# Kernel optimization log

Measured on AMD Instinct MI355X. Metric: run time of the kernel, lower is better.

The kernel has to match this reference:

```python
import jax, jax.numpy as jnp
import numpy as np

B_, C, N, M, DX = 4, 8, 1024, 1024, 1
POINTS_PER_UNIT = 64


def setup_inputs() -> dict:
    key = jax.random.key(0)
    k1, k2, k3 = jax.random.split(key, 3)
    xz = jax.random.uniform(k1, (M, DX), dtype=jnp.float32)          # grid locations
    z = jax.random.normal(k2, (B_, C, M, M), dtype=jnp.float32)      # grid encoding
    x = jax.random.normal(k3, (B_, N, DX), dtype=jnp.float32)        # target locations
    log_scale = jnp.log(jnp.float32(2.0 / POINTS_PER_UNIT))          # learned scalar
    return {"xz": xz, "z": z, "x": x, "log_scale": log_scale}


def reference(xz, z, x, log_scale):
    # pairwise squared distances: (b, n, m)
    dists2 = jnp.sum((x[:, :, None, :] - xz[None, None, :, :]) ** 2, axis=-1)
    # RBF weights
    weights = jnp.exp(-0.5 * dists2 / jnp.exp(2.0 * log_scale))      # (b, n, m)
    # weighted interpolation of grid encoding: (b, c, n, m)
    z1 = jnp.einsum("bnm,bcmk->bcnk", weights, z)
    # outer product z1 @ z1^T: (b, c, n, n)
    z2 = jnp.einsum("bcnk,bcok->bcno", z1, z1)
    return (xz, z2)
```

## Files before the change

kernel.cpp:

```cpp
#include <hip/hip_runtime.h>
#include <hip/hip_bf16.h>


typedef __attribute__((ext_vector_type(8))) unsigned short u16x8;
typedef __attribute__((ext_vector_type(8))) __bf16 bf16x8;
typedef __attribute__((ext_vector_type(4))) float f32x4;

typedef __attribute__((address_space(1))) void gvoid;
typedef __attribute__((address_space(3))) void svoid;
#define GLDS(g, s) __builtin_amdgcn_global_load_lds((gvoid*)(g), (svoid*)(s), 16, 0, 0)
#define BAR() asm volatile("s_barrier" ::: "memory")

__device__ __forceinline__ unsigned short f2bf(float f) {
  unsigned int u = __builtin_bit_cast(unsigned int, f);
  u += 0x7fffu + ((u >> 16) & 1u);
  return (unsigned short)(u >> 16);
}

__device__ __forceinline__ bf16x8 as_bf16x8(u16x8 v) {
  return __builtin_bit_cast(bf16x8, v);
}

__global__ void weights_kernel(const float* __restrict__ xz, const float* __restrict__ x,
                               const float* __restrict__ ls, unsigned short* __restrict__ W) {
  int bn = blockIdx.x;
  float xv = x[bn];
  float coef = -0.5f * __expf(-2.0f * ls[0]);
  unsigned short* Wrow = W + (size_t)bn * 1024;
  #pragma unroll
  for (int i = 0; i < 4; ++i) {
    int m = threadIdx.x + i * 256;
    float d = xv - xz[m];
    Wrow[m] = f2bf(__expf(coef * d * d));
  }
}

__global__ void transpose_kernel(const float* __restrict__ Z, unsigned short* __restrict__ Zt) {
  __shared__ float tile[64][65];
  int bc = blockIdx.z;
  const float* Zp = Z + ((size_t)bc << 20);
  unsigned short* Ztp = Zt + ((size_t)bc << 20);
  int m0 = blockIdx.x * 64, k0 = blockIdx.y * 64;
  int tx = threadIdx.x & 63, tg = threadIdx.x >> 6;
  #pragma unroll
  for (int i = 0; i < 16; ++i) {
    int ml = tg + i * 4;
    tile[ml][tx] = Zp[(size_t)(m0 + ml) * 1024 + k0 + tx];
  }
  __syncthreads();
  int tx2 = (threadIdx.x & 31) * 2, kg = threadIdx.x >> 5;
  #pragma unroll
  for (int i = 0; i < 8; ++i) {
    int kl = kg + i * 8;
    ushort2 v;
    v.x = f2bf(tile[tx2][kl]);
    v.y = f2bf(tile[tx2 + 1][kl]);
    *(ushort2*)&Ztp[(size_t)(k0 + kl) * 1024 + m0 + tx2] = v;
  }
}

template<bool A_PER_B>
__global__ __launch_bounds__(512, 2)
void gemm_nt8(const unsigned short* __restrict__ A, const unsigned short* __restrict__ B,
              unsigned short* __restrict__ Cbf) {
  extern __shared__ __align__(16) char smem[];

  const int bid = blockIdx.x;
  const int w = ((bid & 7) << 6) + (bid >> 3);
  const int bc = w >> 4;
  const int t  = w & 15;
  const int bi = t & 3, bj = t >> 2;

  const unsigned short* Ap = A + ((size_t)(A_PER_B ? (bc >> 3) : bc) << 20);
  const unsigned short* Bp = B + ((size_t)bc << 20);
  const int tid = threadIdx.x;
  const int wv = tid >> 6, lane = tid & 63;
  const int wr = wv >> 2, wc = wv & 3;
  const int la = lane & 15, ha = lane >> 4;

  f32x4 acc[8][4] = {};

  const int slog = (lane & 7) ^ (lane >> 3);
  const int rloc = 2 * (lane >> 3) + (slog & 1);
  const int cloc = (slog >> 1) * 8;
  const unsigned short* gA0 = Ap + (size_t)(bi*256 +       wv*16 + rloc) * 1024 + cloc;
  const unsigned short* gA1 = Ap + (size_t)(bi*256 + 128 + wv*16 + rloc) * 1024 + cloc;
  const unsigned short* gB0 = Bp + (size_t)(bj*256 +       wv*16 + rloc) * 1024 + cloc;
  const unsigned short* gB1 = Bp + (size_t)(bj*256 + 128 + wv*16 + rloc) * 1024 + cloc;
  const int ldsw = wv * 1024;

  auto stageA = [&](int d, int kh, int kt) {
    const int ko = kt * 64 + kh * 32;
    char* dst = smem + d * 32768 + kh * 16384 + ldsw;
    GLDS(gA0 + ko, dst); GLDS(gA1 + ko, dst + 8192);
  };
  auto stageB = [&](int d, int kh, int kt) {
    const int ko = kt * 64 + kh * 32;
    char* dst = smem + 65536 + d * 32768 + kh * 16384 + ldsw;
    GLDS(gB0 + ko, dst); GLDS(gB1 + ko, dst + 8192);
  };

  const int sphys = ((ha << 1) | (la & 1)) ^ (la >> 1);
  const int abase = wr * 8192 + (la >> 1) * 128 + sphys * 16;
  const int bbase = 65536 + wc * 4096 + (la >> 1) * 128 + sphys * 16;

  u16x8 af[4], bfr[4];
  auto lda = [&](int d, int kh, int ms) {
    const char* p = smem + d * 32768 + kh * 16384 + ms * 4096 + abase;
    af[0] = *(const u16x8*)(p);
    af[1] = *(const u16x8*)(p + 1024);
    af[2] = *(const u16x8*)(p + 2048);
    af[3] = *(const u16x8*)(p + 3072);
  };
  auto ldb = [&](int d, int kh) {
    const char* p = smem + d * 32768 + kh * 16384 + bbase;
    bfr[0] = *(const u16x8*)(p);
    bfr[1] = *(const u16x8*)(p + 1024);
    bfr[2] = *(const u16x8*)(p + 2048);
    bfr[3] = *(const u16x8*)(p + 3072);
  };
  auto mfma16 = [&](int ms) {
    __builtin_amdgcn_s_setprio(1);
    #pragma unroll
    for (int i = 0; i < 4; ++i)
      #pragma unroll
      for (int n = 0; n < 4; ++n)
        acc[ms * 4 + i][n] = __builtin_amdgcn_mfma_f32_16x16x32_bf16(
            as_bf16x8(af[i]), as_bf16x8(bfr[n]), acc[ms * 4 + i][n], 0, 0, 0);
    __builtin_amdgcn_s_setprio(0);
  };

  stageA(0, 0, 0); stageB(0, 0, 0);
  stageA(0, 1, 0); stageB(0, 1, 0);
  stageA(1, 0, 1); stageB(1, 0, 1);
  asm volatile("s_waitcnt vmcnt(8)" ::: "memory");
  BAR();

  for (int tt = 0; tt < 16; ++tt) {
    const int d = tt & 1;
    if (tt < 15) stageA(d ^ 1, 1, tt + 1);
    ldb(d, 0); lda(d, 0, 0);
    BAR(); mfma16(0); BAR();
    if (tt < 15) stageB(d ^ 1, 1, tt + 1);
    lda(d, 0, 1);
    BAR(); mfma16(1);
    if (tt < 15) { asm volatile("s_waitcnt vmcnt(8)" ::: "memory"); }
    else         { asm volatile("s_waitcnt vmcnt(0)" ::: "memory"); }
    BAR();
    if (tt < 14) stageA(d, 0, tt + 2);
    ldb(d, 1); lda(d, 1, 0);
    BAR(); mfma16(0); BAR();
    if (tt < 14) stageB(d, 0, tt + 2);
    lda(d, 1, 1);
    BAR(); mfma16(1);
    if (tt < 14)       { asm volatile("s_waitcnt vmcnt(8)" ::: "memory"); }
    else if (tt == 14) { asm volatile("s_waitcnt vmcnt(4)" ::: "memory"); }
    BAR();
  }

  const size_t cb20 = (size_t)bc << 20;
  unsigned short* sE = (unsigned short*)(smem) + wv * 1152;
  const int r2 = lane >> 2, ch = lane & 3;
  #pragma unroll
  for (int mb = 0; mb < 8; ++mb) {
    #pragma unroll
    for (int nb = 0; nb < 4; ++nb)
      #pragma unroll
      for (int j = 0; j < 4; ++j)
        sE[(ha * 4 + j) * 72 + nb * 16 + la] = f2bf(acc[mb][nb][j]);
    u16x8 v0 = *(const u16x8*)&sE[r2 * 72 + ch * 16];
    u16x8 v1 = *(const u16x8*)&sE[r2 * 72 + ch * 16 + 8];
    unsigned short* gp = Cbf + cb20 +
        (size_t)(bi * 256 + wr * 128 + mb * 16 + r2) * 1024 + bj * 256 + wc * 64 + ch * 16;
    *(u16x8*)gp = v0;
    *(u16x8*)(gp + 8) = v1;
  }
}

__global__ __launch_bounds__(256, 3)
void gemm2_sym(const unsigned short* __restrict__ A, float* __restrict__ Cf) {
  __shared__ __align__(16) char smem[49152];

  const int chunk = 144;
  int w = ((int)blockIdx.x & 7) * chunk + ((int)blockIdx.x >> 3);
  int bc = w / 36;
  int t  = w % 36;
  int bi = 0;
  while (t >= 8 - bi) { t -= 8 - bi; ++bi; }
  int bj = bi + t;

  const unsigned short* Ap = A + ((size_t)bc << 20);
  const int tid = threadIdx.x;
  const int wave = tid >> 6, lane = tid & 63;
  const int wr = wave >> 1, wc = wave & 1;
  const int la = lane & 15, ha = lane >> 4;
  f32x4 acc[4][4] = {};

  const int slog = (lane & 7) ^ ((lane >> 3) & 7);
  const int rloc = 2 * (lane >> 3) + (slog & 1);
  const int cloc = (slog >> 1) * 8;
  const unsigned short* gA0 = Ap + (size_t)(bi * 128 + (wave * 2)     * 16 + rloc) * 1024 + cloc;
  const unsigned short* gA1 = Ap + (size_t)(bi * 128 + (wave * 2 + 1) * 16 + rloc) * 1024 + cloc;
  const unsigned short* gB0 = Ap + (size_t)(bj * 128 + (wave * 2)     * 16 + rloc) * 1024 + cloc;
  const unsigned short* gB1 = Ap + (size_t)(bj * 128 + (wave * 2 + 1) * 16 + rloc) * 1024 + cloc;

  auto stage = [&](int slot, int kt) {
    char* dA = smem + slot * 8192 + wave * 2048;
    char* dB = smem + 24576 + slot * 8192 + wave * 2048;
    GLDS(gA0 + kt, dA); GLDS(gA1 + kt, dA + 1024);
    GLDS(gB0 + kt, dB); GLDS(gB1 + kt, dB + 1024);
  };

  const int sphys = ((ha << 1) | (la & 1)) ^ (la >> 1);
  const int aoff = wr * 4096 + (la >> 1) * 128 + sphys * 16;
  const int boff = wc * 4096 + (la >> 1) * 128 + sphys * 16;

  auto compute = [&](int slot) {
    const char* rA = smem + slot * 8192;
    const char* rB = smem + 24576 + slot * 8192;
    u16x8 af[4], bfr[4];
    #pragma unroll
    for (int m = 0; m < 4; ++m) af[m]  = *(const u16x8*)(rA + aoff + m * 1024);
    #pragma unroll
    for (int n = 0; n < 4; ++n) bfr[n] = *(const u16x8*)(rB + boff + n * 1024);
    #pragma unroll
    for (int m = 0; m < 4; ++m)
      #pragma unroll
      for (int n = 0; n < 4; ++n)
        acc[m][n] = __builtin_amdgcn_mfma_f32_16x16x32_bf16(
            as_bf16x8(af[m]), as_bf16x8(bfr[n]), acc[m][n], 0, 0, 0);
  };

  stage(0, 0);
  stage(1, 32);
  asm volatile("s_waitcnt vmcnt(4)" ::: "memory");
  __builtin_amdgcn_s_barrier();
  int sl0 = 0, sl1 = 1, sl2 = 2;
  for (int t2 = 0; t2 < 32; ++t2) {
    if (t2 < 30) stage(sl2, (t2 + 2) * 32);
    compute(sl0);
    if (t2 < 30)       asm volatile("s_waitcnt vmcnt(4)" ::: "memory");
    else if (t2 == 30) asm volatile("s_waitcnt vmcnt(0)" ::: "memory");
    if (t2 < 31) __builtin_amdgcn_s_barrier();
    int tmp = sl0; sl0 = sl1; sl1 = sl2; sl2 = tmp;
  }
  __builtin_amdgcn_s_barrier();

  const size_t cb20 = (size_t)bc << 20;

  #pragma unroll
  for (int m = 0; m < 4; ++m) {
    int row0 = bi * 128 + wr * 64 + m * 16 + ha * 4;
    #pragma unroll
    for (int n = 0; n < 4; ++n) {
      int col = bj * 128 + wc * 64 + n * 16 + la;
      #pragma unroll
      for (int j = 0; j < 4; ++j)
        Cf[cb20 + (size_t)(row0 + j) * 1024 + col] = acc[m][n][j];
    }
  }
  if (bi != bj) {
    float (*sT)[129] = (float(*)[129])smem;
    #pragma unroll
    for (int b = 0; b < 4; ++b) {
      if (wr == (b >> 1)) {
        #pragma unroll
        for (int dm = 0; dm < 2; ++dm) {
          int m = (b & 1) * 2 + dm;
          #pragma unroll
          for (int n = 0; n < 4; ++n)
            #pragma unroll
            for (int j = 0; j < 4; ++j)
              sT[dm * 16 + ha * 4 + j][wc * 64 + n * 16 + la] = acc[m][n][j];
        }
      }
      __syncthreads();
      int c  = tid >> 1;
      int r0 = (tid & 1) * 16;
      float* gp = Cf + cb20 + (size_t)(bj * 128 + c) * 1024 + bi * 128 + b * 32 + r0;
      #pragma unroll
      for (int q = 0; q < 4; ++q) {
        f32x4 v;
        #pragma unroll
        for (int k = 0; k < 4; ++k) v[k] = sT[r0 + q * 4 + k][c];
        *(f32x4*)(gp + q * 4) = v;
      }
      __syncthreads();
    }
  }
}

extern "C" void kernel_launch(void* const* d_in, const int* in_sizes, int n_in,
                              void* d_out, int out_size, void* d_ws, size_t ws_size,
                              hipStream_t stream) {
  const float* xz = (const float*)d_in[0];
  const float* z  = (const float*)d_in[1];
  const float* x  = (const float*)d_in[2];
  const float* ls = (const float*)d_in[3];
  float* out = (float*)d_out;

  unsigned short* W  = (unsigned short*)d_ws;
  unsigned short* Zt = W + ((size_t)4 << 20);
  unsigned short* z1 = Zt + ((size_t)32 << 20);

  hipFuncSetAttribute((const void*)gemm_nt8<true>,
                      hipFuncAttributeMaxDynamicSharedMemorySize, 131072);

  hipMemcpyAsync(out, xz, 1024 * sizeof(float), hipMemcpyDeviceToDevice, stream);
  weights_kernel<<<4096, 256, 0, stream>>>(xz, x, ls, W);
  transpose_kernel<<<dim3(16, 16, 32), 256, 0, stream>>>(z, Zt);
  gemm_nt8<true><<<512, 512, 131072, stream>>>(W, Zt, z1);
  gemm2_sym<<<32 * 36, 256, 0, stream>>>(z1, out + 1024);
}
```

Baseline: 182.7 us.

## Software-pipeline LDS fragment loads with double-buffered registers and fewer barriers

Restructures the GEMM main loop so the A/B fragments for the next MFMA block are read from shared memory into a second register set while the current block computes. This removes about half of the per-step barriers and lets LDS reads overlap with matrix-core work. The last iterations are peeled into an explicit epilogue. The cost is higher register pressure from the doubled fragment registers, plus a possible LDS hazard if a stage overwrites a buffer that is still being read.

Measured after the change: 172.8 us. -5.4%, faster.

```diff
diff --git a/kernel.cpp b/kernel.cpp
--- a/kernel.cpp
+++ b/kernel.cpp
@@ -104,29 +104,29 @@
   const int abase = wr * 8192 + (la >> 1) * 128 + sphys * 16;
   const int bbase = 65536 + wc * 4096 + (la >> 1) * 128 + sphys * 16;
 
-  u16x8 af[4], bfr[4];
-  auto lda = [&](int d, int kh, int ms) {
+  u16x8 aX[4], aY[4], b0[4], b1[4];
+  auto lda4 = [&](u16x8* dst, int d, int kh, int ms) {
     const char* p = smem + d * 32768 + kh * 16384 + ms * 4096 + abase;
-    af[0] = *(const u16x8*)(p);
-    af[1] = *(const u16x8*)(p + 1024);
-    af[2] = *(const u16x8*)(p + 2048);
-    af[3] = *(const u16x8*)(p + 3072);
-  };
-  auto ldb = [&](int d, int kh) {
+    dst[0] = *(const u16x8*)(p);
+    dst[1] = *(const u16x8*)(p + 1024);
+    dst[2] = *(const u16x8*)(p + 2048);
+    dst[3] = *(const u16x8*)(p + 3072);
+  };
+  auto ldb4 = [&](u16x8* dst, int d, int kh) {
     const char* p = smem + d * 32768 + kh * 16384 + bbase;
-    bfr[0] = *(const u16x8*)(p);
-    bfr[1] = *(const u16x8*)(p + 1024);
-    bfr[2] = *(const u16x8*)(p + 2048);
-    bfr[3] = *(const u16x8*)(p + 3072);
-  };
-  auto mfma16 = [&](int ms) {
+    dst[0] = *(const u16x8*)(p);
+    dst[1] = *(const u16x8*)(p + 1024);
+    dst[2] = *(const u16x8*)(p + 2048);
+    dst[3] = *(const u16x8*)(p + 3072);
+  };
+  auto mfma16 = [&](const u16x8* Af, const u16x8* Bf, int ms) {
     __builtin_amdgcn_s_setprio(1);
     #pragma unroll
     for (int i = 0; i < 4; ++i)
       #pragma unroll
       for (int n = 0; n < 4; ++n)
         acc[ms * 4 + i][n] = __builtin_amdgcn_mfma_f32_16x16x32_bf16(
-            as_bf16x8(af[i]), as_bf16x8(bfr[n]), acc[ms * 4 + i][n], 0, 0, 0);
+            as_bf16x8(Af[i]), as_bf16x8(Bf[n]), acc[ms * 4 + i][n], 0, 0, 0);
     __builtin_amdgcn_s_setprio(0);
   };
 
@@ -135,28 +135,51 @@
   stageA(1, 0, 1); stageB(1, 0, 1);
   asm volatile("s_waitcnt vmcnt(8)" ::: "memory");
   BAR();
-
-  for (int tt = 0; tt < 16; ++tt) {
+  ldb4(b0, 0, 0); lda4(aX, 0, 0, 0);
+
+  for (int tt = 0; tt < 14; ++tt) {
     const int d = tt & 1;
-    if (tt < 15) stageA(d ^ 1, 1, tt + 1);
-    ldb(d, 0); lda(d, 0, 0);
-    BAR(); mfma16(0); BAR();
-    if (tt < 15) stageB(d ^ 1, 1, tt + 1);
-    lda(d, 0, 1);
-    BAR(); mfma16(1);
-    if (tt < 15) { asm volatile("s_waitcnt vmcnt(8)" ::: "memory"); }
-    else         { asm volatile("s_waitcnt vmcnt(0)" ::: "memory"); }
+    stageA(d ^ 1, 1, tt + 1);
+    lda4(aY, d, 0, 1);
+    mfma16(aX, b0, 0);
+    stageB(d ^ 1, 1, tt + 1);
+    asm volatile("s_waitcnt vmcnt(8)" ::: "memory");
     BAR();
-    if (tt < 14) stageA(d, 0, tt + 2);
-    ldb(d, 1); lda(d, 1, 0);
-    BAR(); mfma16(0); BAR();
-    if (tt < 14) stageB(d, 0, tt + 2);
-    lda(d, 1, 1);
-    BAR(); mfma16(1);
-    if (tt < 14)       { asm volatile("s_waitcnt vmcnt(8)" ::: "memory"); }
-    else if (tt == 14) { asm volatile("s_waitcnt vmcnt(4)" ::: "memory"); }
+    ldb4(b1, d, 1); lda4(aX, d, 1, 0);
+    mfma16(aY, b0, 1);
+    stageA(d, 0, tt + 2);
+    lda4(aY, d, 1, 1);
+    mfma16(aX, b1, 0);
+    stageB(d, 0, tt + 2);
+    asm volatile("s_waitcnt vmcnt(8)" ::: "memory");
     BAR();
-  }
+    ldb4(b0, d ^ 1, 0); lda4(aX, d ^ 1, 0, 0);
+    mfma16(aY, b1, 1);
+  }
+  stageA(1, 1, 15);
+  lda4(aY, 0, 0, 1);
+  mfma16(aX, b0, 0);
+  stageB(1, 1, 15);
+  asm volatile("s_waitcnt vmcnt(8)" ::: "memory");
+  BAR();
+  ldb4(b1, 0, 1); lda4(aX, 0, 1, 0);
+  mfma16(aY, b0, 1);
+  lda4(aY, 0, 1, 1);
+  mfma16(aX, b1, 0);
+  asm volatile("s_waitcnt vmcnt(4)" ::: "memory");
+  BAR();
+  ldb4(b0, 1, 0); lda4(aX, 1, 0, 0);
+  mfma16(aY, b1, 1);
+  lda4(aY, 1, 0, 1);
+  mfma16(aX, b0, 0);
+  asm volatile("s_waitcnt vmcnt(0)" ::: "memory");
+  BAR();
+  ldb4(b1, 1, 1); lda4(aX, 1, 1, 0);
+  mfma16(aY, b0, 1);
+  lda4(aY, 1, 1, 1);
+  mfma16(aX, b1, 0);
+  mfma16(aY, b1, 1);
+  BAR();
 
   const size_t cb20 = (size_t)bc << 20;
   unsigned short* sE = (unsigned short*)(smem) + wv * 1152;
```
